# Optimization experiments

Hardware: AMD Instinct MI355X
Metric: run time of the kernel (lower is better)

The kernel has to match this reference:

```python
import jax, jax.numpy as jnp
import numpy as np
import math

L = 4      # model_layers
D = 512    # model_filters
H = 32     # heads = max(D//16, 1)
DH = D // H  # 16
S = 1024   # dataset_dimension == max_len == seq_len
B = 2
EPS = 1e-5


def setup_inputs() -> dict:
    key = jax.random.key(0)
    ks = jax.random.split(key, 12)
    scale = 0.02
    n = lambda k, shape: jax.random.normal(k, shape, dtype=jnp.float32) * scale
    return {
        "x": jax.random.normal(ks[0], (B, S), dtype=jnp.float32),
        "Winit": n(ks[1], (D,)),               # init_linear weight (1->D)
        "binit": jnp.zeros((D,), jnp.float32),
        "Wq": n(ks[2], (L, D, D)), "bq": jnp.zeros((L, D), jnp.float32),
        "Wk": n(ks[3], (L, D, D)), "bk": jnp.zeros((L, D), jnp.float32),
        "Wv": n(ks[4], (L, D, D)), "bv": jnp.zeros((L, D), jnp.float32),
        "Er": jax.random.normal(ks[5], (L, S, DH), dtype=jnp.float32) * scale,
        "Wlin": n(ks[6], (L, D, D)), "blin": jnp.zeros((L, D), jnp.float32),
        "ln_g": jnp.ones((L, D), jnp.float32), "ln_b": jnp.zeros((L, D), jnp.float32),
        "Wout": n(ks[7], (D, 1)),              # output_linear, no bias
    }


def layernorm(x, g, b):
    mu = jnp.mean(x, axis=-1, keepdims=True)
    var = jnp.mean(jnp.square(x - mu), axis=-1, keepdims=True)
    return (x - mu) * jax.lax.rsqrt(var + EPS) * g + b


def rel_attn(h, Wq, bq, Wk, bk, Wv, bv, Er):
    # h: [B, S, D]
    b_, s_, _ = h.shape
    q = (h @ Wq + bq).reshape(b_, s_, H, DH).transpose(0, 2, 1, 3)  # [B,H,S,dh]
    k = (h @ Wk + bk).reshape(b_, s_, H, DH).transpose(0, 2, 1, 3)
    v = (h @ Wv + bv).reshape(b_, s_, H, DH).transpose(0, 2, 1, 3)
    # relative-position term with skew trick (seq_len == max_len -> full Er)
    QEr = jnp.einsum('bhsd,td->bhst', q, Er)                  # [B,H,S,S]
    padded = jnp.pad(QEr, ((0, 0), (0, 0), (0, 0), (1, 0)))   # pad left of last dim
    Srel = padded.reshape(b_, H, s_ + 1, s_)[:, :, 1:, :]     # skew
    scores = (jnp.einsum('bhsd,bhtd->bhst', q, k) + Srel) / math.sqrt(DH)
    mask = jnp.tril(jnp.ones((s_, s_), dtype=bool))           # causal
    scores = jnp.where(mask, scores, -jnp.inf)
    p = jax.nn.softmax(scores, axis=-1)
    o = jnp.einsum('bhst,bhtd->bhsd', p, v)
    return o.transpose(0, 2, 1, 3).reshape(b_, s_, D)


def reference(x, Winit, binit, Wq, bq, Wk, bk, Wv, bv, Er, Wlin, blin, ln_g, ln_b, Wout):
    # init_linear(1->D) on scalar per position, then exact gelu
    h = jax.nn.gelu(x[..., None] * Winit + binit, approximate=False)  # [B,S,D]
    for l in range(L):
        a = rel_attn(h, Wq[l], bq[l], Wk[l], bk[l], Wv[l], bv[l], Er[l])
        y = layernorm(a @ Wlin[l] + blin[l], ln_g[l], ln_b[l])
        h = h + jax.nn.gelu(y, approximate=False)
    return h.sum(axis=-2) @ Wout  # [B,1]
```

## Files before the change

### kernel.cpp

```cpp
#include <hip/hip_runtime.h>
#include <math.h>

#define NL 4
#define DIM 512
#define NH 32
#define DHD 16
#define SEQ 1024
#define NB 2
#define LN_EPS 1e-5f
#define NEGF (-1e30f)
#define QSC 0.36067376022224085f

typedef _Float16 half4 __attribute__((ext_vector_type(4)));
typedef _Float16 half8 __attribute__((ext_vector_type(8)));
typedef float floatx4 __attribute__((ext_vector_type(4)));

__device__ __forceinline__ float gelu_exact(float x) {
    return 0.5f * x * (1.0f + erff(x * 0.70710678118654752f));
}

__global__ __launch_bounds__(256) void k_prep_w(const float* __restrict__ Wq,
        const float* __restrict__ Wk, const float* __restrict__ Wv,
        const float* __restrict__ Wlin, _Float16* __restrict__ Wqkvt,
        _Float16* __restrict__ Wlint) {
    __shared__ _Float16 lt[64][72];
    const int mz = blockIdx.z;
    const int l = mz >> 2, which = mz & 3;
    const float* src = (which == 0) ? Wq : (which == 1) ? Wk : (which == 2) ? Wv : Wlin;
    src += (size_t)l * 262144;
    const float scale = (which == 0) ? QSC : 1.0f;
    _Float16* dst = (which < 3) ? (Wqkvt + (size_t)l * 786432 + (size_t)which * 262144)
                                : (Wlint + (size_t)l * 262144);
    const int k0 = blockIdx.x << 6, n0 = blockIdx.y << 6;
    const int tid = threadIdx.x;
    #pragma unroll
    for (int p = 0; p < 4; p++) {
        int kl = (p << 4) + (tid >> 4);
        int n4 = (tid & 15) << 2;
        float4 wv = *(const float4*)(src + (size_t)(k0 + kl) * 512 + n0 + n4);
        lt[n4 + 0][kl] = (_Float16)(wv.x * scale);
        lt[n4 + 1][kl] = (_Float16)(wv.y * scale);
        lt[n4 + 2][kl] = (_Float16)(wv.z * scale);
        lt[n4 + 3][kl] = (_Float16)(wv.w * scale);
    }
    __syncthreads();
    int nl = tid >> 2, k16 = (tid & 3) << 4;
    float4* d4 = (float4*)(dst + (size_t)(n0 + nl) * 512 + k0 + k16);
    const float4* s4 = (const float4*)&lt[nl][k16];
    d4[0] = s4[0];
    d4[1] = s4[1];
}

__global__ __launch_bounds__(256) void k_prep_small(const float* __restrict__ bq,
        const float* __restrict__ bk, const float* __restrict__ bv,
        const float* __restrict__ Er, float* __restrict__ bqkv,
        _Float16* __restrict__ Erh) {
    int idx = blockIdx.x * 256 + threadIdx.x;
    if (idx < NL * 1536) {
        int l = idx / 1536, j = idx % 1536;
        int which = j >> 9, jj = j & 511;
        float val = (which == 0) ? bq[l * 512 + jj] * QSC
                  : (which == 1) ? bk[l * 512 + jj] : bv[l * 512 + jj];
        bqkv[idx] = val;
    }
    int e = idx - NL * 1536;
    if (e >= 0 && e < NL * SEQ * DHD) Erh[e] = (_Float16)Er[e];
}

__global__ __launch_bounds__(256) void k_init(const float* __restrict__ x,
        const float* __restrict__ Wi, const float* __restrict__ bi,
        float* __restrict__ h, _Float16* __restrict__ hf) {
    int idx = blockIdx.x * 256 + threadIdx.x;
    int d = idx & (DIM - 1);
    int bs = idx >> 9;
    float val = gelu_exact(x[bs] * Wi[d] + bi[d]);
    h[idx] = val;
    hf[idx] = (_Float16)val;
}

template<int F16OUT>
__global__ __launch_bounds__(256) void k_gemm_mfma(const _Float16* __restrict__ A,
        const _Float16* __restrict__ Bt, const float* __restrict__ bias,
        _Float16* __restrict__ o16, float* __restrict__ o32) {
    __shared__ _Float16 As[64][72];
    __shared__ _Float16 Bs[128][72];
    const int tid = threadIdx.x;
    const int w = tid >> 6, lane = tid & 63;
    const int wm = (w & 1) << 5;
    const int wn = (w >> 1) << 6;
    const int nn = lane & 15, qd = lane >> 4;
    const int m0 = blockIdx.x << 6, n0 = blockIdx.y << 7;
    floatx4 acc[2][4] = {};
    for (int k0 = 0; k0 < 512; k0 += 64) {
        __syncthreads();
        #pragma unroll
        for (int r = 0; r < 2; r++) {
            int c = tid + (r << 8);
            int row = c >> 3, k8 = (c & 7) << 3;
            *(half8*)&As[row][k8] = *(const half8*)(A + (size_t)(m0 + row) * 512 + k0 + k8);
        }
        #pragma unroll
        for (int r = 0; r < 4; r++) {
            int c = tid + (r << 8);
            int row = c >> 3, k8 = (c & 7) << 3;
            *(half8*)&Bs[row][k8] = *(const half8*)(Bt + (size_t)(n0 + row) * 512 + k0 + k8);
        }
        __syncthreads();
        #pragma unroll
        for (int ks = 0; ks < 2; ks++) {
            half8 af[2], bf[4];
            #pragma unroll
            for (int t = 0; t < 2; t++)
                af[t] = *(const half8*)&As[wm + (t << 4) + nn][(ks << 5) + (qd << 3)];
            #pragma unroll
            for (int t = 0; t < 4; t++)
                bf[t] = *(const half8*)&Bs[wn + (t << 4) + nn][(ks << 5) + (qd << 3)];
            #pragma unroll
            for (int ti = 0; ti < 2; ti++)
                #pragma unroll
                for (int tj = 0; tj < 4; tj++)
                    acc[ti][tj] = __builtin_amdgcn_mfma_f32_16x16x32_f16(
                            af[ti], bf[tj], acc[ti][tj], 0, 0, 0);
        }
    }
    float bv[4];
    #pragma unroll
    for (int tj = 0; tj < 4; tj++) bv[tj] = bias[n0 + wn + (tj << 4) + nn];
    #pragma unroll
    for (int ti = 0; ti < 2; ti++) {
        int rowg = m0 + wm + (ti << 4) + (qd << 2);
        #pragma unroll
        for (int tj = 0; tj < 4; tj++) {
            int colg = n0 + wn + (tj << 4) + nn;
            #pragma unroll
            for (int r = 0; r < 4; r++) {
                float val = acc[ti][tj][r] + bv[tj];
                if (F16OUT) {
                    int which = colg >> 9, ci = colg & 511;
                    o16[(size_t)which * 1048576 + (size_t)(rowg + r) * 512 + ci] = (_Float16)val;
                } else {
                    o32[(size_t)(rowg + r) * 512 + colg] = val;
                }
            }
        }
    }
}

__global__ __launch_bounds__(256) void k_attn_mfma(const _Float16* __restrict__ q,
        const _Float16* __restrict__ k, const _Float16* __restrict__ v,
        const _Float16* __restrict__ Er, _Float16* __restrict__ aout) {
    __shared__ _Float16 Ks[512][20];
    __shared__ _Float16 Vts[16][520];
    __shared__ float Rel[4][16][84];
    const int tid = threadIdx.x;
    const int wid = tid >> 6, lane = tid & 63;
    const int nn = lane & 15, a4 = (lane >> 4) << 2;
    const int b_ = blockIdx.x >> 5, h_ = blockIdx.x & 31;
    const int y = blockIdx.y;
    const int t_ = tid >> 2, c4 = (tid & 3) << 2;
    const int r0p[2] = {64 * y, 64 * (15 - y)};
    const int R = r0p[1] + 64;

    half4 qf[2];
    floatx4 O[2];
    float m[2], lsum[2];
    #pragma unroll
    for (int ph = 0; ph < 2; ph++) {
        int s0w = r0p[ph] + 16 * wid;
        qf[ph] = *(const half4*)(q + ((size_t)(b_ * SEQ + s0w + nn)) * DIM + h_ * DHD + a4);
        O[ph] = (floatx4){0.f, 0.f, 0.f, 0.f};
        m[ph] = NEGF;
        lsum[ph] = 0.f;
    }

    for (int part = 0; part < 2; part++) {
        const int p0 = part << 9;
        if (p0 >= R) break;
        const int pend = (R < p0 + 512) ? R : (p0 + 512);
        __syncthreads();
        const int ng = (pend - p0) >> 6;
        for (int g = 0; g < ng; g++) {
            int rl = (g << 6) + t_;
            size_t gb = ((size_t)(b_ * SEQ + p0 + rl)) * DIM + h_ * DHD + c4;
            *(half4*)&Ks[rl][c4] = *(const half4*)(k + gb);
            half4 vv4 = *(const half4*)(v + gb);
            Vts[c4 + 0][rl] = vv4.x;
            Vts[c4 + 1][rl] = vv4.y;
            Vts[c4 + 2][rl] = vv4.z;
            Vts[c4 + 3][rl] = vv4.w;
        }
        __syncthreads();
        #pragma unroll
        for (int ph = 0; ph < 2; ph++) {
            const int r0 = r0p[ph];
            const int s0w = r0 + 16 * wid;
            const int hi = (r0 + 64 < pend) ? (r0 + 64) : pend;
            for (int ct = p0; ct < hi; ct += 64) {
                const int ctl = ct - p0;
                const int jbw = 1008 - s0w + ct;
                #pragma unroll
                for (int jt = 0; jt < 5; jt++) {
                    int j = jbw + (jt << 4) + nn;
                    j = (j < SEQ - 1) ? j : (SEQ - 1);
                    half4 ef = *(const half4*)(Er + (size_t)j * DHD + a4);
                    floatx4 racc = {0.f, 0.f, 0.f, 0.f};
                    racc = __builtin_amdgcn_mfma_f32_16x16x16f16(ef, qf[ph], racc, 0, 0, 0);
                    *(floatx4*)&Rel[wid][nn][(jt << 4) + a4] = racc;
                }
                float st[4][4];
                const bool diag = (ct == r0);
                #pragma unroll
                for (int tt = 0; tt < 4; tt++) {
                    half4 kf = *(const half4*)&Ks[ctl + (tt << 4) + nn][a4];
                    floatx4 sacc = {0.f, 0.f, 0.f, 0.f};
                    sacc = __builtin_amdgcn_mfma_f32_16x16x16f16(kf, qf[ph], sacc, 0, 0, 0);
                    #pragma unroll
                    for (int r = 0; r < 4; r++) {
                        int tl = (tt << 4) + a4 + r;
                        float sv = sacc[r] + Rel[wid][nn][15 - nn + tl];
                        if (diag && (tl > 16 * wid + nn)) sv = NEGF;
                        st[tt][r] = sv;
                    }
                }
                float cmax = NEGF;
                #pragma unroll
                for (int tt = 0; tt < 4; tt++)
                    #pragma unroll
                    for (int r = 0; r < 4; r++) cmax = fmaxf(cmax, st[tt][r]);
                cmax = fmaxf(cmax, __shfl_xor(cmax, 16));
                cmax = fmaxf(cmax, __shfl_xor(cmax, 32));
                float mnew = fmaxf(m[ph], cmax);
                float alpha = exp2f(m[ph] - mnew);
                m[ph] = mnew;
                float csum = 0.f;
                half4 pf[4];
                #pragma unroll
                for (int tt = 0; tt < 4; tt++) {
                    float p0e = exp2f(st[tt][0] - mnew);
                    float p1e = exp2f(st[tt][1] - mnew);
                    float p2e = exp2f(st[tt][2] - mnew);
                    float p3e = exp2f(st[tt][3] - mnew);
                    csum += (p0e + p1e) + (p2e + p3e);
                    half4 ph4 = {(_Float16)p0e, (_Float16)p1e, (_Float16)p2e, (_Float16)p3e};
                    pf[tt] = ph4;
                }
                csum += __shfl_xor(csum, 16);
                csum += __shfl_xor(csum, 32);
                lsum[ph] = lsum[ph] * alpha + csum;
                O[ph][0] *= alpha; O[ph][1] *= alpha; O[ph][2] *= alpha; O[ph][3] *= alpha;
                #pragma unroll
                for (int tt = 0; tt < 4; tt++) {
                    half4 vf = *(const half4*)&Vts[nn][ctl + (tt << 4) + a4];
                    O[ph] = __builtin_amdgcn_mfma_f32_16x16x16f16(vf, pf[tt], O[ph], 0, 0, 0);
                }
            }
        }
    }
    #pragma unroll
    for (int ph = 0; ph < 2; ph++) {
        float linv = 1.0f / lsum[ph];
        int s0w = r0p[ph] + 16 * wid;
        half4 ov = { (_Float16)(O[ph][0] * linv), (_Float16)(O[ph][1] * linv),
                     (_Float16)(O[ph][2] * linv), (_Float16)(O[ph][3] * linv) };
        *(half4*)(aout + ((size_t)(b_ * SEQ + s0w + nn)) * DIM + h_ * DHD + a4) = ov;
    }
}

__global__ __launch_bounds__(256) void k_ln_gelu_res(const float* __restrict__ y,
        const float* __restrict__ gam, const float* __restrict__ bet,
        float* __restrict__ h, _Float16* __restrict__ hf) {
    __shared__ float red[8];
    int row = blockIdx.x, tid = threadIdx.x;
    const float* yr = y + (size_t)row * DIM;
    float v0 = yr[tid], v1 = yr[tid + 256];
    float sum = v0 + v1, sq = v0 * v0 + v1 * v1;
    #pragma unroll
    for (int off = 32; off > 0; off >>= 1) {
        sum += __shfl_down(sum, off);
        sq  += __shfl_down(sq, off);
    }
    if ((tid & 63) == 0) { red[tid >> 6] = sum; red[4 + (tid >> 6)] = sq; }
    __syncthreads();
    float ts = red[0] + red[1] + red[2] + red[3];
    float tq = red[4] + red[5] + red[6] + red[7];
    float mu = ts * (1.0f / DIM);
    float var = tq * (1.0f / DIM) - mu * mu;
    float rs = rsqrtf(var + LN_EPS);
    float z0 = (v0 - mu) * rs * gam[tid] + bet[tid];
    float z1 = (v1 - mu) * rs * gam[tid + 256] + bet[tid + 256];
    size_t base = (size_t)row * DIM;
    float nh0 = h[base + tid] + gelu_exact(z0);
    float nh1 = h[base + tid + 256] + gelu_exact(z1);
    h[base + tid] = nh0;
    h[base + tid + 256] = nh1;
    hf[base + tid] = (_Float16)nh0;
    hf[base + tid + 256] = (_Float16)nh1;
}

__global__ __launch_bounds__(256) void k_colsum(const float* __restrict__ h,
        float* __restrict__ partial) {
    int bt = blockIdx.x;
    int b_ = bt >> 4, t = bt & 15;
    int tid = threadIdx.x;
    #pragma unroll
    for (int half = 0; half < 2; half++) {
        int d = half * 256 + tid;
        float acc = 0.f;
        for (int i = 0; i < 64; i++)
            acc += h[((size_t)(b_ * SEQ + t * 64 + i)) * DIM + d];
        partial[(size_t)bt * DIM + d] = acc;
    }
}

__global__ __launch_bounds__(256) void k_final(const float* __restrict__ partial,
        const float* __restrict__ Wout, float* __restrict__ out) {
    __shared__ float red[4][2];
    int tid = threadIdx.x;
    float acc0 = 0.f, acc1 = 0.f;
    #pragma unroll
    for (int half = 0; half < 2; half++) {
        int d = half * 256 + tid;
        float w = Wout[d];
        float s0 = 0.f, s1 = 0.f;
        for (int t = 0; t < 16; t++) {
            s0 += partial[t * DIM + d];
            s1 += partial[(16 + t) * DIM + d];
        }
        acc0 += s0 * w;
        acc1 += s1 * w;
    }
    #pragma unroll
    for (int off = 32; off > 0; off >>= 1) {
        acc0 += __shfl_down(acc0, off);
        acc1 += __shfl_down(acc1, off);
    }
    if ((tid & 63) == 0) { red[tid >> 6][0] = acc0; red[tid >> 6][1] = acc1; }
    __syncthreads();
    if (tid == 0) {
        out[0] = red[0][0] + red[1][0] + red[2][0] + red[3][0];
        out[1] = red[0][1] + red[1][1] + red[2][1] + red[3][1];
    }
}

extern "C" void kernel_launch(void* const* d_in, const int* in_sizes, int n_in,
                              void* d_out, int out_size, void* d_ws, size_t ws_size,
                              hipStream_t stream) {
    const float* x    = (const float*)d_in[0];
    const float* Wi   = (const float*)d_in[1];
    const float* bi   = (const float*)d_in[2];
    const float* Wq   = (const float*)d_in[3];
    const float* bq   = (const float*)d_in[4];
    const float* Wk   = (const float*)d_in[5];
    const float* bk   = (const float*)d_in[6];
    const float* Wv   = (const float*)d_in[7];
    const float* bv   = (const float*)d_in[8];
    const float* Er   = (const float*)d_in[9];
    const float* Wlin = (const float*)d_in[10];
    const float* blin = (const float*)d_in[11];
    const float* lng  = (const float*)d_in[12];
    const float* lnb  = (const float*)d_in[13];
    const float* Wout = (const float*)d_in[14];
    float* out = (float*)d_out;

    float* ws = (float*)d_ws;
    const size_t N1 = 1048576;
    float*     h     = ws;
    _Float16*  hf    = (_Float16*)(ws + N1);
    _Float16*  qh    = (_Float16*)(ws + N1 + N1/2);
    float*     y     = ws + N1 + N1/2;
    _Float16*  ah    = (_Float16*)(ws + 3 * N1);
    _Float16*  Wqkvt = (_Float16*)(ws + 3 * N1 + N1/2);
    _Float16*  Wlint = (_Float16*)(ws + 5 * N1);
    float*     bqkv  = ws + 5 * N1 + N1/2;
    _Float16*  Erh   = (_Float16*)(ws + 5 * N1 + N1/2 + 8192);
    float*     pa    = ws + 5 * N1 + N1/2 + 8192 + 32768;

    k_prep_w<<<dim3(8, 8, 16), dim3(256), 0, stream>>>(Wq, Wk, Wv, Wlin, Wqkvt, Wlint);
    k_prep_small<<<dim3(280), dim3(256), 0, stream>>>(bq, bk, bv, Er, bqkv, Erh);
    k_init<<<dim3(4096), dim3(256), 0, stream>>>(x, Wi, bi, h, hf);
    for (int l = 0; l < NL; l++) {
        k_gemm_mfma<1><<<dim3(32, 12), dim3(256), 0, stream>>>(
                hf, Wqkvt + (size_t)l * 786432, bqkv + l * 1536, qh, nullptr);
        k_attn_mfma<<<dim3(NB * NH, 8), dim3(256), 0, stream>>>(
                qh, qh + 1048576, qh + 2097152, Erh + (size_t)l * 16384, ah);
        k_gemm_mfma<0><<<dim3(32, 4), dim3(256), 0, stream>>>(
                ah, Wlint + (size_t)l * 262144, blin + l * 512, nullptr, y);
        k_ln_gelu_res<<<dim3(NB * SEQ), dim3(256), 0, stream>>>(
                y, lng + l * 512, lnb + l * 512, h, hf);
    }
    k_colsum<<<dim3(32), dim3(256), 0, stream>>>(h, pa);
    k_final<<<dim3(1), dim3(256), 0, stream>>>(pa, Wout, out);
}
```

Before: 327.4 us.

## Split attention over key ranges with merge kernel and shrink GEMM tile

Attention drops the paired-query-tile load balancing and instead launches one block per query tile and key-split half (16x2 grid per head). Each half writes unnormalised fp32 outputs plus running max and sum, and a new merge kernel combines them with log-sum-exp weights. The GEMM tile shrinks from 64x128 to 64x64 to double block count. The intent is more parallelism and occupancy, at the cost of an extra kernel launch, fp32 partial-output traffic and less reuse per GEMM block.

```diff
diff --git a/kernel.cpp b/kernel.cpp
--- a/kernel.cpp
+++ b/kernel.cpp
@@ -83,14 +83,14 @@
         const _Float16* __restrict__ Bt, const float* __restrict__ bias,
         _Float16* __restrict__ o16, float* __restrict__ o32) {
     __shared__ _Float16 As[64][72];
-    __shared__ _Float16 Bs[128][72];
+    __shared__ _Float16 Bs[64][72];
     const int tid = threadIdx.x;
     const int w = tid >> 6, lane = tid & 63;
     const int wm = (w & 1) << 5;
-    const int wn = (w >> 1) << 6;
+    const int wn = (w >> 1) << 5;
     const int nn = lane & 15, qd = lane >> 4;
-    const int m0 = blockIdx.x << 6, n0 = blockIdx.y << 7;
-    floatx4 acc[2][4] = {};
+    const int m0 = blockIdx.x << 6, n0 = blockIdx.y << 6;
+    floatx4 acc[2][2] = {};
     for (int k0 = 0; k0 < 512; k0 += 64) {
         __syncthreads();
         #pragma unroll
@@ -98,39 +98,33 @@
             int c = tid + (r << 8);
             int row = c >> 3, k8 = (c & 7) << 3;
             *(half8*)&As[row][k8] = *(const half8*)(A + (size_t)(m0 + row) * 512 + k0 + k8);
-        }
-        #pragma unroll
-        for (int r = 0; r < 4; r++) {
-            int c = tid + (r << 8);
-            int row = c >> 3, k8 = (c & 7) << 3;
             *(half8*)&Bs[row][k8] = *(const half8*)(Bt + (size_t)(n0 + row) * 512 + k0 + k8);
         }
         __syncthreads();
         #pragma unroll
         for (int ks = 0; ks < 2; ks++) {
-            half8 af[2], bf[4];
-            #pragma unroll
-            for (int t = 0; t < 2; t++)
+            half8 af[2], bf[2];
+            #pragma unroll
+            for (int t = 0; t < 2; t++) {
                 af[t] = *(const half8*)&As[wm + (t << 4) + nn][(ks << 5) + (qd << 3)];
-            #pragma unroll
-            for (int t = 0; t < 4; t++)
                 bf[t] = *(const half8*)&Bs[wn + (t << 4) + nn][(ks << 5) + (qd << 3)];
+            }
             #pragma unroll
             for (int ti = 0; ti < 2; ti++)
                 #pragma unroll
-                for (int tj = 0; tj < 4; tj++)
+                for (int tj = 0; tj < 2; tj++)
                     acc[ti][tj] = __builtin_amdgcn_mfma_f32_16x16x32_f16(
                             af[ti], bf[tj], acc[ti][tj], 0, 0, 0);
         }
     }
-    float bv[4];
-    #pragma unroll
-    for (int tj = 0; tj < 4; tj++) bv[tj] = bias[n0 + wn + (tj << 4) + nn];
+    float bv[2];
+    #pragma unroll
+    for (int tj = 0; tj < 2; tj++) bv[tj] = bias[n0 + wn + (tj << 4) + nn];
     #pragma unroll
     for (int ti = 0; ti < 2; ti++) {
         int rowg = m0 + wm + (ti << 4) + (qd << 2);
         #pragma unroll
-        for (int tj = 0; tj < 4; tj++) {
+        for (int tj = 0; tj < 2; tj++) {
             int colg = n0 + wn + (tj << 4) + nn;
             #pragma unroll
             for (int r = 0; r < 4; r++) {
@@ -146,42 +140,35 @@
     }
 }
 
-__global__ __launch_bounds__(256) void k_attn_mfma(const _Float16* __restrict__ q,
+__global__ __launch_bounds__(256, 4) void k_attn_mfma(const _Float16* __restrict__ q,
         const _Float16* __restrict__ k, const _Float16* __restrict__ v,
-        const _Float16* __restrict__ Er, _Float16* __restrict__ aout) {
-    __shared__ _Float16 Ks[512][20];
-    __shared__ _Float16 Vts[16][520];
+        const _Float16* __restrict__ Er, float* __restrict__ Osp,
+        float* __restrict__ ml) {
+    __shared__ _Float16 Ks[256][20];
+    __shared__ _Float16 Vts[16][264];
     __shared__ float Rel[4][16][84];
     const int tid = threadIdx.x;
     const int wid = tid >> 6, lane = tid & 63;
     const int nn = lane & 15, a4 = (lane >> 4) << 2;
     const int b_ = blockIdx.x >> 5, h_ = blockIdx.x & 31;
-    const int y = blockIdx.y;
+    const int qt = blockIdx.y, sp = blockIdx.z;
+    const int nch = qt + 1;
+    const int hsp = (nch + 1) >> 1;
+    const int c_lo = sp ? hsp : 0, c_hi = sp ? nch : hsp;
+    const int r0 = qt << 6;
+    const int s0w = r0 + (wid << 4);
     const int t_ = tid >> 2, c4 = (tid & 3) << 2;
-    const int r0p[2] = {64 * y, 64 * (15 - y)};
-    const int R = r0p[1] + 64;
-
-    half4 qf[2];
-    floatx4 O[2];
-    float m[2], lsum[2];
-    #pragma unroll
-    for (int ph = 0; ph < 2; ph++) {
-        int s0w = r0p[ph] + 16 * wid;
-        qf[ph] = *(const half4*)(q + ((size_t)(b_ * SEQ + s0w + nn)) * DIM + h_ * DHD + a4);
-        O[ph] = (floatx4){0.f, 0.f, 0.f, 0.f};
-        m[ph] = NEGF;
-        lsum[ph] = 0.f;
-    }
-
-    for (int part = 0; part < 2; part++) {
-        const int p0 = part << 9;
-        if (p0 >= R) break;
-        const int pend = (R < p0 + 512) ? R : (p0 + 512);
+
+    half4 qf = *(const half4*)(q + ((size_t)(b_ * SEQ + s0w + nn)) * DIM + h_ * DHD + a4);
+    floatx4 O = {0.f, 0.f, 0.f, 0.f};
+    float m = NEGF, lsum = 0.f;
+
+    for (int cg = c_lo; cg < c_hi; cg += 4) {
+        const int cge = (cg + 4 < c_hi) ? (cg + 4) : c_hi;
         __syncthreads();
-        const int ng = (pend - p0) >> 6;
-        for (int g = 0; g < ng; g++) {
+        for (int g = 0; g < cge - cg; g++) {
             int rl = (g << 6) + t_;
-            size_t gb = ((size_t)(b_ * SEQ + p0 + rl)) * DIM + h_ * DHD + c4;
+            size_t gb = ((size_t)(b_ * SEQ + (cg << 6) + rl)) * DIM + h_ * DHD + c4;
             *(half4*)&Ks[rl][c4] = *(const half4*)(k + gb);
             half4 vv4 = *(const half4*)(v + gb);
             Vts[c4 + 0][rl] = vv4.x;
@@ -190,80 +177,96 @@
             Vts[c4 + 3][rl] = vv4.w;
         }
         __syncthreads();
-        #pragma unroll
-        for (int ph = 0; ph < 2; ph++) {
-            const int r0 = r0p[ph];
-            const int s0w = r0 + 16 * wid;
-            const int hi = (r0 + 64 < pend) ? (r0 + 64) : pend;
-            for (int ct = p0; ct < hi; ct += 64) {
-                const int ctl = ct - p0;
-                const int jbw = 1008 - s0w + ct;
+        for (int c = cg; c < cge; c++) {
+            const int ct = c << 6;
+            const int ctl = (c - cg) << 6;
+            const int jbw = 1008 - s0w + ct;
+            #pragma unroll
+            for (int jt = 0; jt < 5; jt++) {
+                int j = jbw + (jt << 4) + nn;
+                j = (j < SEQ - 1) ? j : (SEQ - 1);
+                half4 ef = *(const half4*)(Er + (size_t)j * DHD + a4);
+                floatx4 racc = {0.f, 0.f, 0.f, 0.f};
+                racc = __builtin_amdgcn_mfma_f32_16x16x16f16(ef, qf, racc, 0, 0, 0);
+                *(floatx4*)&Rel[wid][nn][(jt << 4) + a4] = racc;
+            }
+            float st[4][4];
+            const bool diag = (ct == r0);
+            #pragma unroll
+            for (int tt = 0; tt < 4; tt++) {
+                half4 kf = *(const half4*)&Ks[ctl + (tt << 4) + nn][a4];
+                floatx4 sacc = {0.f, 0.f, 0.f, 0.f};
+                sacc = __builtin_amdgcn_mfma_f32_16x16x16f16(kf, qf, sacc, 0, 0, 0);
                 #pragma unroll
-                for (int jt = 0; jt < 5; jt++) {
-                    int j = jbw + (jt << 4) + nn;
-                    j = (j < SEQ - 1) ? j : (SEQ - 1);
-                    half4 ef = *(const half4*)(Er + (size_t)j * DHD + a4);
-                    floatx4 racc = {0.f, 0.f, 0.f, 0.f};
-                    racc = __builtin_amdgcn_mfma_f32_16x16x16f16(ef, qf[ph], racc, 0, 0, 0);
-                    *(floatx4*)&Rel[wid][nn][(jt << 4) + a4] = racc;
+                for (int r = 0; r < 4; r++) {
+                    int tl = (tt << 4) + a4 + r;
+                    float sv = sacc[r] + Rel[wid][nn][15 - nn + tl];
+                    if (diag && (tl > (wid << 4) + nn)) sv = NEGF;
+                    st[tt][r] = sv;
                 }
-                float st[4][4];
-                const bool diag = (ct == r0);
+            }
+            float cmax = NEGF;
+            #pragma unroll
+            for (int tt = 0; tt < 4; tt++)
                 #pragma unroll
-                for (int tt = 0; tt < 4; tt++) {
-                    half4 kf = *(const half4*)&Ks[ctl + (tt << 4) + nn][a4];
-                    floatx4 sacc = {0.f, 0.f, 0.f, 0.f};
-                    sacc = __builtin_amdgcn_mfma_f32_16x16x16f16(kf, qf[ph], sacc, 0, 0, 0);
-                    #pragma unroll
-                    for (int r = 0; r < 4; r++) {
-                        int tl = (tt << 4) + a4 + r;
-                        float sv = sacc[r] + Rel[wid][nn][15 - nn + tl];
-                        if (diag && (tl > 16 * wid + nn)) sv = NEGF;
-                        st[tt][r] = sv;
-                    }
-                }
-                float cmax = NEGF;
-                #pragma unroll
-                for (int tt = 0; tt < 4; tt++)
-                    #pragma unroll
-                    for (int r = 0; r < 4; r++) cmax = fmaxf(cmax, st[tt][r]);
-                cmax = fmaxf(cmax, __shfl_xor(cmax, 16));
-                cmax = fmaxf(cmax, __shfl_xor(cmax, 32));
-                float mnew = fmaxf(m[ph], cmax);
-                float alpha = exp2f(m[ph] - mnew);
-                m[ph] = mnew;
-                float csum = 0.f;
-                half4 pf[4];
-                #pragma unroll
-                for (int tt = 0; tt < 4; tt++) {
-                    float p0e = exp2f(st[tt][0] - mnew);
-                    float p1e = exp2f(st[tt][1] - mnew);
-                    float p2e = exp2f(st[tt][2] - mnew);
-                    float p3e = exp2f(st[tt][3] - mnew);
-                    csum += (p0e + p1e) + (p2e + p3e);
-                    half4 ph4 = {(_Float16)p0e, (_Float16)p1e, (_Float16)p2e, (_Float16)p3e};
-                    pf[tt] = ph4;
-                }
-                csum += __shfl_xor(csum, 16);
-                csum += __shfl_xor(csum, 32);
-                lsum[ph] = lsum[ph] * alpha + csum;
-                O[ph][0] *= alpha; O[ph][1] *= alpha; O[ph][2] *= alpha; O[ph][3] *= alpha;
-                #pragma unroll
-                for (int tt = 0; tt < 4; tt++) {
-                    half4 vf = *(const half4*)&Vts[nn][ctl + (tt << 4) + a4];
-                    O[ph] = __builtin_amdgcn_mfma_f32_16x16x16f16(vf, pf[tt], O[ph], 0, 0, 0);
-                }
-            }
-        }
-    }
-    #pragma unroll
-    for (int ph = 0; ph < 2; ph++) {
-        float linv = 1.0f / lsum[ph];
-        int s0w = r0p[ph] + 16 * wid;
-        half4 ov = { (_Float16)(O[ph][0] * linv), (_Float16)(O[ph][1] * linv),
-                     (_Float16)(O[ph][2] * linv), (_Float16)(O[ph][3] * linv) };
-        *(half4*)(aout + ((size_t)(b_ * SEQ + s0w + nn)) * DIM + h_ * DHD + a4) = ov;
-    }
+                for (int r = 0; r < 4; r++) cmax = fmaxf(cmax, st[tt][r]);
+            cmax = fmaxf(cmax, __shfl_xor(cmax, 16));
+            cmax = fmaxf(cmax, __shfl_xor(cmax, 32));
+            float mnew = fmaxf(m, cmax);
+            float alpha = exp2f(m - mnew);
+            m = mnew;
+            float csum = 0.f;
+            half4 pf[4];
+            #pragma unroll
+            for (int tt = 0; tt < 4; tt++) {
+                float p0e = exp2f(st[tt][0] - mnew);
+                float p1e = exp2f(st[tt][1] - mnew);
+                float p2e = exp2f(st[tt][2] - mnew);
+                float p3e = exp2f(st[tt][3] - mnew);
+                csum += (p0e + p1e) + (p2e + p3e);
+                half4 ph4 = {(_Float16)p0e, (_Float16)p1e, (_Float16)p2e, (_Float16)p3e};
+                pf[tt] = ph4;
+            }
+            csum += __shfl_xor(csum, 16);
+            csum += __shfl_xor(csum, 32);
+            lsum = lsum * alpha + csum;
+            O[0] *= alpha; O[1] *= alpha; O[2] *= alpha; O[3] *= alpha;
+            #pragma unroll
+            for (int tt = 0; tt < 4; tt++) {
+                half4 vf = *(const half4*)&Vts[nn][ctl + (tt << 4) + a4];
+                O = __builtin_amdgcn_mfma_f32_16x16x16f16(vf, pf[tt], O, 0, 0, 0);
+            }
+        }
+    }
+    float* op = Osp + (size_t)sp * 1048576
+              + ((size_t)(b_ * SEQ + s0w + nn)) * DIM + h_ * DHD + a4;
+    *(float4*)op = make_float4(O[0], O[1], O[2], O[3]);
+    if (a4 == 0) {
+        float2* mlp = (float2*)ml;
+        mlp[((size_t)((sp * NB + b_) * NH + h_)) * SEQ + s0w + nn] = make_float2(m, lsum);
+    }
+}
+
+__global__ __launch_bounds__(256) void k_attn_merge(const float* __restrict__ Osp,
+        const float* __restrict__ ml, _Float16* __restrict__ ah) {
+    int idx = blockIdx.x * 256 + threadIdx.x;
+    int d4g = (idx & 127) << 2;
+    int row = idx >> 7;
+    int b = row >> 10, s = row & 1023, h = d4g >> 4;
+    const float2* mlp = (const float2*)ml;
+    float2 ml0 = mlp[((size_t)((0 * NB + b) * NH + h)) * SEQ + s];
+    float2 ml1 = mlp[((size_t)((1 * NB + b) * NH + h)) * SEQ + s];
+    float ms = fmaxf(ml0.x, ml1.x);
+    float w0 = exp2f(ml0.x - ms), w1 = exp2f(ml1.x - ms);
+    float li = ml0.y * w0 + ml1.y * w1;
+    float inv = 1.0f / li;
+    float4 O0 = *(const float4*)(Osp + (size_t)row * 512 + d4g);
+    float4 O1 = *(const float4*)(Osp + 1048576 + (size_t)row * 512 + d4g);
+    half4 r = { (_Float16)((O0.x * w0 + O1.x * w1) * inv),
+                (_Float16)((O0.y * w0 + O1.y * w1) * inv),
+                (_Float16)((O0.z * w0 + O1.z * w1) * inv),
+                (_Float16)((O0.w * w0 + O1.w * w1) * inv) };
+    *(half4*)(ah + (size_t)row * 512 + d4g) = r;
 }
 
 __global__ __launch_bounds__(256) void k_ln_gelu_res(const float* __restrict__ y,
@@ -367,23 +370,26 @@
     float*     h     = ws;
     _Float16*  hf    = (_Float16*)(ws + N1);
     _Float16*  qh    = (_Float16*)(ws + N1 + N1/2);
-    float*     y     = ws + N1 + N1/2;
-    _Float16*  ah    = (_Float16*)(ws + 3 * N1);
-    _Float16*  Wqkvt = (_Float16*)(ws + 3 * N1 + N1/2);
-    _Float16*  Wlint = (_Float16*)(ws + 5 * N1);
-    float*     bqkv  = ws + 5 * N1 + N1/2;
-    _Float16*  Erh   = (_Float16*)(ws + 5 * N1 + N1/2 + 8192);
-    float*     pa    = ws + 5 * N1 + N1/2 + 8192 + 32768;
+    float*     y     = ws + 3 * N1;
+    _Float16*  ah    = (_Float16*)(ws + 4 * N1);
+    _Float16*  Wqkvt = (_Float16*)(ws + 4 * N1 + N1/2);
+    _Float16*  Wlint = (_Float16*)(ws + 6 * N1);
+    float*     bqkv  = ws + 6 * N1 + N1/2;
+    _Float16*  Erh   = (_Float16*)(ws + 6 * N1 + N1/2 + 8192);
+    float*     Osp   = ws + 7 * N1;
+    float*     ml    = ws + 9 * N1;
+    float*     pa    = ws + 9 * N1 + 262144 + 64;
 
     k_prep_w<<<dim3(8, 8, 16), dim3(256), 0, stream>>>(Wq, Wk, Wv, Wlin, Wqkvt, Wlint);
     k_prep_small<<<dim3(280), dim3(256), 0, stream>>>(bq, bk, bv, Er, bqkv, Erh);
     k_init<<<dim3(4096), dim3(256), 0, stream>>>(x, Wi, bi, h, hf);
     for (int l = 0; l < NL; l++) {
-        k_gemm_mfma<1><<<dim3(32, 12), dim3(256), 0, stream>>>(
+        k_gemm_mfma<1><<<dim3(32, 24), dim3(256), 0, stream>>>(
                 hf, Wqkvt + (size_t)l * 786432, bqkv + l * 1536, qh, nullptr);
-        k_attn_mfma<<<dim3(NB * NH, 8), dim3(256), 0, stream>>>(
-                qh, qh + 1048576, qh + 2097152, Erh + (size_t)l * 16384, ah);
-        k_gemm_mfma<0><<<dim3(32, 4), dim3(256), 0, stream>>>(
+        k_attn_mfma<<<dim3(NB * NH, 16, 2), dim3(256), 0, stream>>>(
+                qh, qh + 1048576, qh + 2097152, Erh + (size_t)l * 16384, Osp, ml);
+        k_attn_merge<<<dim3(1024), dim3(256), 0, stream>>>(Osp, ml, ah);
+        k_gemm_mfma<0><<<dim3(32, 8), dim3(256), 0, stream>>>(
                 ah, Wlint + (size_t)l * 262144, blin + l * 512, nullptr, y);
         k_ln_gelu_res<<<dim3(NB * SEQ), dim3(256), 0, stream>>>(
                 y, lng + l * 512, lnb + l * 512, h, hf);
```

Measured after the change: 322.3 us. No clear change (-1.6%).
